# Optimization experiments

Hardware: AMD Instinct MI355X
Metric: run time of the kernel (lower is better)

## Reference

```python
import jax, jax.numpy as jnp
import numpy as np

B = 8
C = 256
N40, N20, N10 = 1600, 400, 100
N = N40 + N20 + N10  # 2100 pixel nodes (40x40 + 20x20 + 10x10)

def _grid_edges(h, w, off):
    # 8-neighborhood 'contextual' edges within one scale's grid
    idx = np.arange(h * w).reshape(h, w)
    srcs, dsts = [], []
    for di in (-1, 0, 1):
        for dj in (-1, 0, 1):
            if di == 0 and dj == 0:
                continue
            s = idx[max(0, -di):h - max(0, di), max(0, -dj):w - max(0, dj)]
            d = idx[max(0, di):h - max(0, -di), max(0, dj):w - max(0, -dj)]
            srcs.append(off + s.ravel())
            dsts.append(off + d.ravel())
    return srcs, dsts

def _hier_edges(ph, pw, poff, coff):
    # bidirected parent <-> 4-children 'hierarchical' edges between scales
    i, j = np.meshgrid(np.arange(ph), np.arange(pw), indexing='ij')
    parent = (poff + i * pw + j).ravel()
    srcs, dsts = [], []
    cw = 2 * pw
    for di in (0, 1):
        for dj in (0, 1):
            child = (coff + (2 * i + di) * cw + (2 * j + dj)).ravel()
            srcs += [parent, child]
            dsts += [child, parent]
    return srcs, dsts

def build_edges():
    loop = [np.arange(N)]  # dgl.add_self_loop on both etypes
    cs, cd = [], []
    for (h, w, off) in ((40, 40, 0), (20, 20, N40), (10, 10, N40 + N20)):
        s, d = _grid_edges(h, w, off)
        cs += s; cd += d
    ctx_src = np.concatenate(cs + loop); ctx_dst = np.concatenate(cd + loop)
    hs, hd = [], []
    s, d = _hier_edges(20, 20, N40, 0); hs += s; hd += d
    s, d = _hier_edges(10, 10, N40 + N20, N40); hs += s; hd += d
    hier_src = np.concatenate(hs + loop); hier_dst = np.concatenate(hd + loop)
    return (jnp.asarray(ctx_src, jnp.int32), jnp.asarray(ctx_dst, jnp.int32),
            jnp.asarray(hier_src, jnp.int32), jnp.asarray(hier_dst, jnp.int32))

def _bn_relu(x, g, b, m, v):
    # inference-mode BatchNorm2d + ReLU
    scale = g * jax.lax.rsqrt(v + 1e-5)
    return jax.nn.relu(x * scale[:, None, None] + (b - m * scale)[:, None, None])

def _conv1x1(x, w, b):
    return jnp.einsum('bchw,oc->bohw', x, w) + b[:, None, None]

def _avgpool2(x):
    b, c, h, w = x.shape
    return x.reshape(b, c, h // 2, 2, w // 2, 2).mean(axis=(3, 5))

def _up2(x):
    return jnp.repeat(jnp.repeat(x, 2, axis=2), 2, axis=3)

def _gnn(h, src, dst, deg_inv, w, b):
    # gather -> scatter-add -> mean over in-neighbors (incl. self loop) -> linear -> ReLU
    agg = jnp.zeros_like(h).at[:, dst].add(h[:, src]) * deg_inv[None, :, None]
    return jax.nn.relu(jnp.einsum('bnc,cd->bnd', agg, w) + b)

def _convT2x2(x, wt, b):
    # stride-2 2x2 transposed conv; wt: [Cin, Cout, 2, 2] (torch layout)
    bsz, cin, h, w = x.shape
    y = jnp.einsum('bchw,cokl->bohkwl', x, wt)
    return y.reshape(bsz, wt.shape[1], 2 * h, 2 * w) + b[:, None, None]

def setup_inputs():
    key = jax.random.key(0)
    ks = iter(jax.random.split(key, 64))
    def rn(shape, scale=0.02):
        return jax.random.normal(next(ks), shape, jnp.float32) * scale
    inp = {}
    inp['feat0'] = rn((B, 256, 160, 160), 1.0)
    inp['feat1'] = rn((B, 512, 80, 80), 1.0)
    inp['feat2'] = rn((B, 1024, 40, 40), 1.0)
    inp['feat3'] = rn((B, 2048, 20, 20), 1.0)
    for i, cin in ((1, 512), (2, 1024), (3, 2048)):
        inp['dw%d' % i] = rn((256, cin))
        inp['db%d' % i] = jnp.zeros((256,), jnp.float32)
        inp['g%d' % i] = jnp.ones((256,), jnp.float32)
        inp['b%d' % i] = jnp.zeros((256,), jnp.float32)
        inp['m%d' % i] = jnp.zeros((256,), jnp.float32)
        inp['v%d' % i] = jnp.ones((256,), jnp.float32)
    for i in range(1, 7):
        inp['gW%d' % i] = rn((256, 256))
        inp['gb%d' % i] = jnp.zeros((256,), jnp.float32)
    for i, cout in ((1, 512), (2, 1024), (3, 2048)):
        inp['tW%d' % i] = rn((256, cout, 2, 2))
        inp['tb%d' % i] = jnp.zeros((cout,), jnp.float32)
    ctx_src, ctx_dst, hier_src, hier_dst = build_edges()
    inp['ctx_src'] = ctx_src; inp['ctx_dst'] = ctx_dst
    inp['hier_src'] = hier_src; inp['hier_dst'] = hier_dst
    return inp

def reference(feat0, feat1, feat2, feat3,
              dw1, db1, g1, b1, m1, v1,
              dw2, db2, g2, b2, m2, v2,
              dw3, db3, g3, b3, m3, v3,
              gW1, gb1, gW2, gb2, gW3, gb3, gW4, gb4, gW5, gb5, gW6, gb6,
              tW1, tb1, tW2, tb2, tW3, tb3,
              ctx_src, ctx_dst, hier_src, hier_dst):
    f40 = _avgpool2(_bn_relu(_conv1x1(feat1, dw1, db1), g1, b1, m1, v1))  # [B,256,40,40]
    f20 = _avgpool2(_bn_relu(_conv1x1(feat2, dw2, db2), g2, b2, m2, v2))  # [B,256,20,20]
    f10 = _avgpool2(_bn_relu(_conv1x1(feat3, dw3, db3), g3, b3, m3, v3))  # [B,256,10,10]
    bsz = f40.shape[0]
    # cnn_gnn: flatten all three scales into [B, 2100, 256] node features (batched
    # version of the original per-sample python loop; graph is identical per sample)
    h = jnp.concatenate([
        f40.reshape(bsz, C, N40).transpose(0, 2, 1),
        f20.reshape(bsz, C, N20).transpose(0, 2, 1),
        f10.reshape(bsz, C, N10).transpose(0, 2, 1)], axis=1)
    dic = 1.0 / jnp.zeros((N,), h.dtype).at[ctx_dst].add(1.0)
    dih = 1.0 / jnp.zeros((N,), h.dtype).at[hier_dst].add(1.0)
    # context1, context2, hierarch1, hierarch2, context4, context5
    h = _gnn(h, ctx_src, ctx_dst, dic, gW1, gb1)
    h = _gnn(h, ctx_src, ctx_dst, dic, gW2, gb2)
    h = _gnn(h, hier_src, hier_dst, dih, gW3, gb3)
    h = _gnn(h, hier_src, hier_dst, dih, gW4, gb4)
    h = _gnn(h, ctx_src, ctx_dst, dic, gW5, gb5)
    h = _gnn(h, ctx_src, ctx_dst, dic, gW6, gb6)
    # gnn_cnn: split back to NCHW maps
    f40g = h[:, :N40].transpose(0, 2, 1).reshape(bsz, C, 40, 40)
    f20g = h[:, N40:N40 + N20].transpose(0, 2, 1).reshape(bsz, C, 20, 20)
    f10g = h[:, N40 + N20:].transpose(0, 2, 1).reshape(bsz, C, 10, 10)
    f10_ref = f10 + f10g
    f20_ref = f20 + f20g + _up2(f10g)
    f40_ref = f40 + f40g + _up2(f20g)
    out1 = _convT2x2(f40_ref, tW1, tb1) + feat1
    out2 = _convT2x2(f20_ref, tW2, tb2) + feat2
    out3 = _convT2x2(f10_ref, tW3, tb3) + feat3
    return (feat0, out1, out2, out3)
```

## Files before the change

### kernel.cpp

```cpp
#include <hip/hip_runtime.h>
#include <cstdint>

#define NODES 2100

typedef __attribute__((ext_vector_type(8))) __bf16 bf16x8;
typedef __attribute__((ext_vector_type(4))) float f32x4;
typedef __attribute__((ext_vector_type(8))) unsigned short u16x8;

__device__ inline float bf2f(unsigned short s) { return __uint_as_float(((unsigned)s) << 16); }
__device__ inline unsigned short f2bf(float f) {
    unsigned u = __float_as_uint(f);
    u += 0x7fff + ((u >> 16) & 1);
    return (unsigned short)(u >> 16);
}
__device__ inline void gload16(const unsigned short* g, void* lds) {
    __builtin_amdgcn_global_load_lds(
        (const __attribute__((address_space(1))) void*)g,
        (__attribute__((address_space(3))) void*)lds, 16, 0, 0);
}

__device__ __attribute__((always_inline)) inline
void gemm_core(const unsigned short* __restrict__ A, const unsigned short* __restrict__ B,
               int K, int m0, int n0, int mClamp, int nClamp,
               unsigned short* As, unsigned short* Bs, f32x4 acc[4][4])
{
    const int t = threadIdx.x, lane = t & 63, w = t >> 6;
    const int wr = w >> 1, wc = w & 1;
    const int sx = (lane & 7) << 4;
    for (int k0 = 0; k0 < K; k0 += 64) {
#pragma unroll
        for (int i = 0; i < 4; ++i) {
            int LO  = ((i << 8) + t) << 4;
            int row = LO >> 7;
            int kb  = (LO & 127) ^ ((row & 7) << 4);
            int ke  = kb >> 1;
            int ra = m0 + row; if (ra > mClamp) ra = mClamp;
            int rb = n0 + row; if (rb > nClamp) rb = nClamp;
            gload16(A + (size_t)ra * K + k0 + ke, (char*)As + LO);
            gload16(B + (size_t)rb * K + k0 + ke, (char*)Bs + LO);
        }
        asm volatile("s_waitcnt vmcnt(0)" ::: "memory");
        __syncthreads();
#pragma unroll
        for (int kk = 0; kk < 2; ++kk) {
            bf16x8 a[4], bb[4];
#pragma unroll
            for (int f = 0; f < 4; ++f) {
                int pa = (((wr * 64 + f * 16 + (lane & 15)) << 7) + kk * 64 + ((lane >> 4) << 4)) ^ sx;
                int pb = (((wc * 64 + f * 16 + (lane & 15)) << 7) + kk * 64 + ((lane >> 4) << 4)) ^ sx;
                a[f]  = *(const bf16x8*)((const char*)As + pa);
                bb[f] = *(const bf16x8*)((const char*)Bs + pb);
            }
#pragma unroll
            for (int fr = 0; fr < 4; ++fr)
#pragma unroll
                for (int fc = 0; fc < 4; ++fc)
                    acc[fr][fc] = __builtin_amdgcn_mfma_f32_16x16x32_bf16(a[fr], bb[fc], acc[fr][fc], 0, 0, 0);
        }
        __syncthreads();
    }
}

struct PrepArgs {
    const float *dw0, *dw1, *dw2;
    const float *gw0, *gw1, *gw2, *gw3, *gw4, *gw5;
    const float *tw0, *tw1, *tw2;
    const float *g0, *g1, *g2, *b0, *b1, *b2, *m0, *m1, *m2, *v0, *v1, *v2, *db0, *db1, *db2;
    unsigned short *dwb, *gWTb, *tWTb;
    float *scshb;
};

__device__ inline void transpose32(const float* __restrict__ in, unsigned short* __restrict__ outT,
                                   int Ccols, int c0, int r0)
{
    __shared__ float T[32][33];
    const int tx = threadIdx.x & 31, ty = threadIdx.x >> 5;
#pragma unroll
    for (int i = 0; i < 4; ++i)
        T[ty + i * 8][tx] = in[(size_t)(r0 + ty + i * 8) * Ccols + c0 + tx];
    __syncthreads();
#pragma unroll
    for (int i = 0; i < 4; ++i)
        outT[(size_t)(c0 + ty + i * 8) * 256 + r0 + tx] = f2bf(T[tx][ty + i * 8]);
}

__global__ __launch_bounds__(256)
void mega_prep(PrepArgs a)
{
    const int bid = blockIdx.x, t = threadIdx.x;
    if (bid < 448) {
        int idx = (bid * 256 + t) * 8;
        const float* src;
        int loc;
        if (idx < 131072)      { src = a.dw0; loc = idx; }
        else if (idx < 393216) { src = a.dw1; loc = idx - 131072; }
        else                   { src = a.dw2; loc = idx - 393216; }
        float4 x = *(const float4*)(src + loc);
        float4 y = *(const float4*)(src + loc + 4);
        u16x8 r;
        r[0] = f2bf(x.x); r[1] = f2bf(x.y); r[2] = f2bf(x.z); r[3] = f2bf(x.w);
        r[4] = f2bf(y.x); r[5] = f2bf(y.y); r[6] = f2bf(y.z); r[7] = f2bf(y.w);
        *(u16x8*)(a.dwb + idx) = r;
    } else if (bid < 832) {
        int gid = bid - 448;
        int l = gid >> 6, sb = gid & 63;
        const float* gw[6] = {a.gw0, a.gw1, a.gw2, a.gw3, a.gw4, a.gw5};
        transpose32(gw[l], a.gWTb + (size_t)l * 65536, 256, (sb & 7) << 5, (sb >> 3) << 5);
    } else if (bid < 4416) {
        int gid = bid - 832;
        const float* tw; unsigned short* dst; int ncx, loc;
        if (gid < 512)       { tw = a.tw0; dst = a.tWTb;           ncx = 64;  loc = gid; }
        else if (gid < 1536) { tw = a.tw1; dst = a.tWTb + 524288;  ncx = 128; loc = gid - 512; }
        else                 { tw = a.tw2; dst = a.tWTb + 1572864; ncx = 256; loc = gid - 1536; }
        int cx = loc % ncx, ry = loc / ncx;
        transpose32(tw, dst, ncx * 32, cx << 5, ry << 5);
    } else {
        const float* g[3]  = {a.g0, a.g1, a.g2};
        const float* b[3]  = {a.b0, a.b1, a.b2};
        const float* m[3]  = {a.m0, a.m1, a.m2};
        const float* v[3]  = {a.v0, a.v1, a.v2};
        const float* db[3] = {a.db0, a.db1, a.db2};
        for (int s = 0; s < 3; ++s) {
            float sc = g[s][t] * rsqrtf(v[s][t] + 1e-5f);
            a.scshb[s * 512 + t] = sc;
            a.scshb[s * 512 + 256 + t] = (db[s][t] - m[s][t]) * sc + b[s][t];
        }
    }
}

struct ConvArgs {
    const float* feat[3];
    const unsigned short* dwb[3];
    const float* scsh[3];
    unsigned short* h0out;
};

__global__ __launch_bounds__(256)
void conv_fused(ConvArgs ca)
{
    __shared__ __align__(16) unsigned short As[64 * 64];
    __shared__ __align__(16) unsigned short Bs[256 * 64];
    int bx = blockIdx.x;
    int s, mt;
    if (bx < 800)       { s = 0; mt = bx; }
    else if (bx < 1000) { s = 1; mt = bx - 800; }
    else                { s = 2; mt = bx - 1000; }
    const int Kc[3]  = {512, 1024, 2048};
    const int Wc[3]  = {80, 40, 20};
    const int PPc[3] = {1600, 400, 100};
    const int nfc[3] = {0, 1600, 2000};
    const int K = Kc[s], W = Wc[s], W2 = W >> 1, HW = W * W, PP = PPc[s], noff = nfc[s];
    const float* feat = ca.feat[s];
    const unsigned short* dw = ca.dwb[s];
    const float* scsh = ca.scsh[s];

    const int t = threadIdx.x, lane = t & 63, w = t >> 6;
    const int sx = (lane & 7) << 4;

    const int ml = t & 63;
    const int kw = t >> 6;
    const int graw = mt * 64 + ml;
    const int b = graw / HW;
    const int rem = graw - b * HW;
    const int pooled = rem >> 2, sub = rem & 3;
    const int pi = pooled / W2, pj = pooled - pi * W2;
    const int i = pi * 2 + (sub >> 1), j = pj * 2 + (sub & 1);
    const float* src = feat + (size_t)b * K * HW + (size_t)i * W + j;
    const int sxm = (ml & 7) << 3;

    f32x4 acc[4][4];
#pragma unroll
    for (int fr = 0; fr < 4; ++fr)
#pragma unroll
        for (int fc = 0; fc < 4; ++fc) acc[fr][fc] = (f32x4){0.f, 0.f, 0.f, 0.f};

    for (int k0 = 0; k0 < K; k0 += 64) {
#pragma unroll
        for (int it = 0; it < 8; ++it) {
            int LO = ((it << 8) + t) << 4;
            int row = LO >> 7;
            int kb = (LO & 127) ^ ((row & 7) << 4);
            gload16(dw + (size_t)row * K + k0 + (kb >> 1), (char*)Bs + LO);
        }
        float v[16];
#pragma unroll
        for (int it = 0; it < 16; ++it)
            v[it] = src[(size_t)(k0 + it * 4 + kw) * HW];
#pragma unroll
        for (int it = 0; it < 16; ++it) {
            int k_l = it * 4 + kw;
            As[(ml << 6) + (k_l ^ sxm)] = f2bf(v[it]);
        }
        asm volatile("s_waitcnt vmcnt(0)" ::: "memory");
        __syncthreads();
#pragma unroll
        for (int kk = 0; kk < 2; ++kk) {
            bf16x8 a[4], bb[4];
#pragma unroll
            for (int f = 0; f < 4; ++f) {
                int pa = (((f * 16 + (lane & 15)) << 7) + kk * 64 + ((lane >> 4) << 4)) ^ sx;
                int pb = (((w * 64 + f * 16 + (lane & 15)) << 7) + kk * 64 + ((lane >> 4) << 4)) ^ sx;
                a[f]  = *(const bf16x8*)((const char*)As + pa);
                bb[f] = *(const bf16x8*)((const char*)Bs + pb);
            }
#pragma unroll
            for (int fr = 0; fr < 4; ++fr)
#pragma unroll
                for (int fc = 0; fc < 4; ++fc)
                    acc[fr][fc] = __builtin_amdgcn_mfma_f32_16x16x32_bf16(a[fr], bb[fc], acc[fr][fc], 0, 0, 0);
        }
        __syncthreads();
    }

#pragma unroll
    for (int fc = 0; fc < 4; ++fc) {
        const int o = w * 64 + fc * 16 + (lane & 15);
        const float sc = scsh[o], sh = scsh[256 + o];
#pragma unroll
        for (int fr = 0; fr < 4; ++fr) {
            const int mrow = mt * 64 + fr * 16 + (lane >> 4) * 4;
            const int q = mrow >> 2;
            const int bi = q / PP;
            const int node = noff + (q - bi * PP);
            float sum = 0.f;
#pragma unroll
            for (int r = 0; r < 4; ++r)
                sum += fmaxf(acc[fr][fc][r] * sc + sh, 0.f);
            ca.h0out[((size_t)(bi * NODES + node)) * 256 + o] = f2bf(sum * 0.25f);
        }
    }
}

__global__ __launch_bounds__(256)
void gnn_fused(const unsigned short* __restrict__ h, const unsigned short* __restrict__ BT,
               const float* __restrict__ bias, unsigned short* __restrict__ out, int hier)
{
    __shared__ __align__(16) unsigned short As[32 * 64];
    __shared__ __align__(16) unsigned short Bs[256 * 64];
    const int t = threadIdx.x, lane = t & 63, w = t >> 6;
    const int r0 = blockIdx.x << 5;
    const int myrow = t >> 3, q = t & 7;
    const int grow = r0 + myrow;
    const int b = grow / NODES;
    const int n = grow - b * NODES;

    int gw, off;
    if (n < 1600)      { gw = 40; off = 0; }
    else if (n < 2000) { gw = 20; off = 1600; }
    else               { gw = 10; off = 2000; }
    const int li = (n - off) / gw;
    const int lj = (n - off) - li * gw;
    int nbr[9]; int cnt = 0;
    if (!hier) {
#pragma unroll
        for (int di = -1; di <= 1; ++di)
#pragma unroll
            for (int dj = -1; dj <= 1; ++dj) {
                int ii = li + di, jj = lj + dj;
                if (ii >= 0 && ii < gw && jj >= 0 && jj < gw) nbr[cnt++] = off + ii * gw + jj;
            }
    } else {
        nbr[cnt++] = n;
        if (off == 0) {
            nbr[cnt++] = 1600 + (li >> 1) * 20 + (lj >> 1);
        } else if (off == 1600) {
            nbr[cnt++] = 2000 + (li >> 1) * 10 + (lj >> 1);
#pragma unroll
            for (int di = 0; di < 2; ++di)
#pragma unroll
                for (int dj = 0; dj < 2; ++dj)
                    nbr[cnt++] = ((li << 1) + di) * 40 + ((lj << 1) + dj);
        } else {
#pragma unroll
            for (int di = 0; di < 2; ++di)
#pragma unroll
                for (int dj = 0; dj < 2; ++dj)
                    nbr[cnt++] = 1600 + ((li << 1) + di) * 20 + ((lj << 1) + dj);
        }
    }
    int nboff[9];
#pragma unroll
    for (int e = 0; e < 9; ++e)
        nboff[e] = (b * NODES + nbr[e < cnt ? e : 0]) * 256 + q * 8;
    const float inv = 1.0f / (float)cnt;
    const int sx = (lane & 7) << 4;
    const int awr = (myrow << 6) + ((q ^ (myrow & 7)) << 3);

    f32x4 acc[2][4];
#pragma unroll
    for (int fr = 0; fr < 2; ++fr)
#pragma unroll
        for (int fc = 0; fc < 4; ++fc) acc[fr][fc] = (f32x4){0.f, 0.f, 0.f, 0.f};

    for (int k0 = 0; k0 < 256; k0 += 64) {
#pragma unroll
        for (int it = 0; it < 8; ++it) {
            int LO = ((it << 8) + t) << 4;
            int row = LO >> 7;
            int kb = (LO & 127) ^ ((row & 7) << 4);
            gload16(BT + (size_t)row * 256 + k0 + (kb >> 1), (char*)Bs + LO);
        }
        float sacc[8] = {0, 0, 0, 0, 0, 0, 0, 0};
        for (int e = 0; e < cnt; ++e) {
            u16x8 vv = *(const u16x8*)(h + nboff[e] + k0);
#pragma unroll
            for (int jj = 0; jj < 8; ++jj) sacc[jj] += bf2f(vv[jj]);
        }
        u16x8 o0;
#pragma unroll
        for (int jj = 0; jj < 8; ++jj) o0[jj] = f2bf(sacc[jj] * inv);
        *(u16x8*)&As[awr] = o0;

        asm volatile("s_waitcnt vmcnt(0)" ::: "memory");
        __syncthreads();
#pragma unroll
        for (int kk = 0; kk < 2; ++kk) {
            bf16x8 a[2], bb[4];
#pragma unroll
            for (int f = 0; f < 2; ++f) {
                int pa = (((f * 16 + (lane & 15)) << 7) + kk * 64 + ((lane >> 4) << 4)) ^ sx;
                a[f] = *(const bf16x8*)((const char*)As + pa);
            }
#pragma unroll
            for (int f = 0; f < 4; ++f) {
                int pb = (((w * 64 + f * 16 + (lane & 15)) << 7) + kk * 64 + ((lane >> 4) << 4)) ^ sx;
                bb[f] = *(const bf16x8*)((const char*)Bs + pb);
            }
#pragma unroll
            for (int fr = 0; fr < 2; ++fr)
#pragma unroll
                for (int fc = 0; fc < 4; ++fc)
                    acc[fr][fc] = __builtin_amdgcn_mfma_f32_16x16x32_bf16(a[fr], bb[fc], acc[fr][fc], 0, 0, 0);
        }
        __syncthreads();
    }

#pragma unroll
    for (int fc = 0; fc < 4; ++fc) {
        const int d = w * 64 + fc * 16 + (lane & 15);
        const float bv = bias[d];
#pragma unroll
        for (int fr = 0; fr < 2; ++fr) {
            int rb = r0 + fr * 16 + (lane >> 4) * 4;
#pragma unroll
            for (int r = 0; r < 4; ++r)
                out[(size_t)(rb + r) * 256 + d] = f2bf(fmaxf(acc[fr][fc][r] + bv, 0.f));
        }
    }
}

__global__ __launch_bounds__(256)
void a_build(const unsigned short* __restrict__ h0, const unsigned short* __restrict__ h6,
             unsigned short* __restrict__ Ao)
{
    int bx = blockIdx.x;
    int P, H2, noff, pbase, pw, haspar; size_t aoff;
    if (bx < 1600)      { P = 1600; H2 = 40; noff = 0;    pbase = 1600; pw = 20; haspar = 1; aoff = 0; }
    else if (bx < 2000) { P = 400;  H2 = 20; noff = 1600; pbase = 2000; pw = 10; haspar = 1; aoff = 12800ULL * 256; bx -= 1600; }
    else                { P = 100;  H2 = 10; noff = 2000; pbase = 0;    pw = 0;  haspar = 0; aoff = 16000ULL * 256; bx -= 2000; }
    const int gid = bx * 256 + threadIdx.x;
    const int m = gid >> 5, c0 = (gid & 31) << 3;
    const int b = m / P, pix = m - b * P;
    const size_t src = ((size_t)(b * NODES + noff + pix)) * 256 + c0;
    u16x8 x0 = *(const u16x8*)(h0 + src);
    u16x8 x6 = *(const u16x8*)(h6 + src);
    float v[8];
#pragma unroll
    for (int e = 0; e < 8; ++e) v[e] = bf2f(x0[e]) + bf2f(x6[e]);
    if (haspar) {
        int ii = pix / H2, jj = pix - ii * H2;
        size_t sp = ((size_t)(b * NODES + pbase + (ii >> 1) * pw + (jj >> 1))) * 256 + c0;
        u16x8 xp = *(const u16x8*)(h6 + sp);
#pragma unroll
        for (int e = 0; e < 8; ++e) v[e] += bf2f(xp[e]);
    }
    u16x8 r;
#pragma unroll
    for (int e = 0; e < 8; ++e) r[e] = f2bf(v[e]);
    *(u16x8*)(Ao + aoff + (size_t)m * 256 + c0) = r;
}

struct ConvtArgs {
    const unsigned short* WT[3];
    const unsigned short* Apix[3];
    const float* tb[3];
    const float* feat[3];
    float* out[3];
};

__global__ __launch_bounds__(256)
void convt_fused(ConvtArgs ct)
{
    __shared__ __align__(16) unsigned short As[8192], Bs[8192];
    int bx = blockIdx.x;
    int s, px, my;
    if (bx < 1600)      { s = 0; px = bx % 100; my = bx / 100; }
    else if (bx < 2400) { s = 1; bx -= 1600; px = bx % 25; my = bx / 25; }
    else                { s = 2; bx -= 2400; px = bx % 7;  my = bx / 7; }
    const int Pc[3]  = {1600, 400, 100};
    const int H2c[3] = {40, 20, 10};
    const int Cc[3]  = {512, 1024, 2048};
    const int Mc[3]  = {12800, 3200, 800};
    const int P = Pc[s], H2 = H2c[s], Cout = Cc[s], Mpix = Mc[s];
    const int m0 = my << 7, n0 = px << 7;

    f32x4 acc[4][4];
#pragma unroll
    for (int fr = 0; fr < 4; ++fr)
#pragma unroll
        for (int fc = 0; fc < 4; ++fc) acc[fr][fc] = (f32x4){0.f, 0.f, 0.f, 0.f};

    gemm_core(ct.WT[s], ct.Apix[s], 256, m0, n0, Cout * 4 - 1, Mpix - 1, As, Bs, acc);

    const int lane = threadIdx.x & 63, w = threadIdx.x >> 6;
    const int wr = w >> 1, wc = w & 1;
    const int H = H2 * 2;
    const float* feat = ct.feat[s];
    float* out = ct.out[s];
#pragma unroll
    for (int fc = 0; fc < 4; ++fc) {
        const int p_g = n0 + wc * 64 + fc * 16 + (lane & 15);
        if (p_g < Mpix) {
            const int b = p_g / P, pix = p_g - b * P;
            const int ii = pix / H2, jj = pix - ii * H2;
#pragma unroll
            for (int fr = 0; fr < 4; ++fr) {
                const int rb = m0 + wr * 64 + fr * 16 + (lane >> 4) * 4;
                const int o = rb >> 2;
                const float tbo = ct.tb[s][o];
                size_t base = (((size_t)(b * Cout + o)) * H + 2 * ii) * H + 2 * jj;
                float2 f0 = *(const float2*)&feat[base];
                float2 r0v; r0v.x = acc[fr][fc][0] + tbo + f0.x; r0v.y = acc[fr][fc][1] + tbo + f0.y;
                *(float2*)&out[base] = r0v;
                float2 f1 = *(const float2*)&feat[base + H];
                float2 r1v; r1v.x = acc[fr][fc][2] + tbo + f1.x; r1v.y = acc[fr][fc][3] + tbo + f1.y;
                *(float2*)&out[base + H] = r1v;
            }
        }
    }
}

extern "C" void kernel_launch(void* const* d_in, const int* in_sizes, int n_in,
                              void* d_out, int out_size, void* d_ws, size_t ws_size,
                              hipStream_t stream)
{
    const float* feats[3] = { (const float*)d_in[1], (const float*)d_in[2], (const float*)d_in[3] };
    const float* gb[6];
    for (int l = 0; l < 6; ++l) gb[l] = (const float*)d_in[23 + 2 * l];
    const float* tb[3] = { (const float*)d_in[35], (const float*)d_in[37], (const float*)d_in[39] };

    size_t off = 0;
    auto alloc = [&](size_t bytes) { size_t r = off; off = (off + bytes + 511) & ~(size_t)511; return r; };
    unsigned short* h0b  = (unsigned short*)((char*)d_ws + alloc(16800ULL * 256 * 2));
    unsigned short* hA   = (unsigned short*)((char*)d_ws + alloc(16800ULL * 256 * 2));
    unsigned short* hB   = (unsigned short*)((char*)d_ws + alloc(16800ULL * 256 * 2));
    unsigned short* dwb  = (unsigned short*)((char*)d_ws + alloc(917504ULL * 2));
    unsigned short* gWTb = (unsigned short*)((char*)d_ws + alloc(6ULL * 65536 * 2));
    unsigned short* tWTb = (unsigned short*)((char*)d_ws + alloc(3670016ULL * 2));
    float*          scshb= (float*)((char*)d_ws + alloc(3ULL * 512 * 4));
    unsigned short* Aconvt = (unsigned short*)((char*)d_ws + off);

    hipMemcpyAsync(d_out, d_in[0], 52428800ULL * 4, hipMemcpyDeviceToDevice, stream);

    PrepArgs pa;
    pa.dw0 = (const float*)d_in[4];  pa.dw1 = (const float*)d_in[10]; pa.dw2 = (const float*)d_in[16];
    pa.gw0 = (const float*)d_in[22]; pa.gw1 = (const float*)d_in[24]; pa.gw2 = (const float*)d_in[26];
    pa.gw3 = (const float*)d_in[28]; pa.gw4 = (const float*)d_in[30]; pa.gw5 = (const float*)d_in[32];
    pa.tw0 = (const float*)d_in[34]; pa.tw1 = (const float*)d_in[36]; pa.tw2 = (const float*)d_in[38];
    pa.g0 = (const float*)d_in[6];  pa.g1 = (const float*)d_in[12]; pa.g2 = (const float*)d_in[18];
    pa.b0 = (const float*)d_in[7];  pa.b1 = (const float*)d_in[13]; pa.b2 = (const float*)d_in[19];
    pa.m0 = (const float*)d_in[8];  pa.m1 = (const float*)d_in[14]; pa.m2 = (const float*)d_in[20];
    pa.v0 = (const float*)d_in[9];  pa.v1 = (const float*)d_in[15]; pa.v2 = (const float*)d_in[21];
    pa.db0 = (const float*)d_in[5]; pa.db1 = (const float*)d_in[11]; pa.db2 = (const float*)d_in[17];
    pa.dwb = dwb; pa.gWTb = gWTb; pa.tWTb = tWTb; pa.scshb = scshb;
    mega_prep<<<dim3(4417), dim3(256), 0, stream>>>(pa);

    ConvArgs ca;
    ca.feat[0] = feats[0]; ca.feat[1] = feats[1]; ca.feat[2] = feats[2];
    ca.dwb[0] = dwb; ca.dwb[1] = dwb + 131072; ca.dwb[2] = dwb + 393216;
    ca.scsh[0] = scshb; ca.scsh[1] = scshb + 512; ca.scsh[2] = scshb + 1024;
    ca.h0out = h0b;
    conv_fused<<<dim3(1050), dim3(256), 0, stream>>>(ca);

    const int types[6] = {0, 0, 1, 1, 0, 0};
    const unsigned short* hin = h0b;
    unsigned short* houts[6] = {hA, hB, hA, hB, hA, hB};
    for (int l = 0; l < 6; ++l) {
        gnn_fused<<<dim3(525), dim3(256), 0, stream>>>(hin, gWTb + (size_t)l * 65536, gb[l], houts[l], types[l]);
        hin = houts[l];
    }
    unsigned short* h6 = hB;

    a_build<<<dim3(2100), dim3(256), 0, stream>>>(h0b, h6, Aconvt);

    ConvtArgs ct;
    ct.WT[0] = tWTb; ct.WT[1] = tWTb + 524288; ct.WT[2] = tWTb + 1572864;
    ct.Apix[0] = Aconvt; ct.Apix[1] = Aconvt + 12800ULL * 256; ct.Apix[2] = Aconvt + 16000ULL * 256;
    ct.tb[0] = tb[0]; ct.tb[1] = tb[1]; ct.tb[2] = tb[2];
    ct.feat[0] = feats[0]; ct.feat[1] = feats[1]; ct.feat[2] = feats[2];
    ct.out[0] = (float*)d_out + 52428800;
    ct.out[1] = (float*)d_out + 52428800 + 26214400;
    ct.out[2] = (float*)d_out + 52428800 + 26214400 + 13107200;
    convt_fused<<<dim3(2848), dim3(256), 0, stream>>>(ct);
}
```

Measured before the change: 500.4 us.

## Split feat0 passthrough copy across compute kernels and prefetch GNN neighbor rows

Replaces the 200MB device-to-device memcpy with eight 26MB chunks, each copied by extra blocks prepended to the prep, conv and six GNN kernels. The aim is to hide the bandwidth-bound copy behind compute-bound or latency-bound kernels instead of running it serially. The GNN kernel also prefetches all nine neighbor vectors for the next K-slice into registers before the MFMA loop, overlapping gather latency with compute. The cost is extra register pressure and copy blocks that compete for memory bandwidth and CUs with the existing work.

```diff
diff --git a/kernel.cpp b/kernel.cpp
--- a/kernel.cpp
+++ b/kernel.cpp
@@ -17,6 +17,12 @@
     __builtin_amdgcn_global_load_lds(
         (const __attribute__((address_space(1))) void*)g,
         (__attribute__((address_space(3))) void*)lds, 16, 0, 0);
+}
+
+__device__ inline void copy_chunk(const float4* __restrict__ s, float4* __restrict__ d,
+                                  int nquads, int bid, int nb)
+{
+    for (int i = bid * 256 + threadIdx.x; i < nquads; i += nb * 256) d[i] = s[i];
 }
 
 __device__ __attribute__((always_inline)) inline
@@ -68,6 +74,7 @@
     const float *g0, *g1, *g2, *b0, *b1, *b2, *m0, *m1, *m2, *v0, *v1, *v2, *db0, *db1, *db2;
     unsigned short *dwb, *gWTb, *tWTb;
     float *scshb;
+    const float4 *cps; float4 *cpd;
 };
 
 __device__ inline void transpose32(const float* __restrict__ in, unsigned short* __restrict__ outT,
@@ -87,7 +94,10 @@
 __global__ __launch_bounds__(256)
 void mega_prep(PrepArgs a)
 {
-    const int bid = blockIdx.x, t = threadIdx.x;
+    int bid = blockIdx.x;
+    const int t = threadIdx.x;
+    if (bid < 512) { copy_chunk(a.cps, a.cpd, 1638400, bid, 512); return; }
+    bid -= 512;
     if (bid < 448) {
         int idx = (bid * 256 + t) * 8;
         const float* src;
@@ -133,6 +143,7 @@
     const unsigned short* dwb[3];
     const float* scsh[3];
     unsigned short* h0out;
+    const float4 *cps; float4 *cpd;
 };
 
 __global__ __launch_bounds__(256)
@@ -141,6 +152,8 @@
     __shared__ __align__(16) unsigned short As[64 * 64];
     __shared__ __align__(16) unsigned short Bs[256 * 64];
     int bx = blockIdx.x;
+    if (bx < 128) { copy_chunk(ca.cps, ca.cpd, 1638400, bx, 128); return; }
+    bx -= 128;
     int s, mt;
     if (bx < 800)       { s = 0; mt = bx; }
     else if (bx < 1000) { s = 1; mt = bx - 800; }
@@ -233,12 +246,16 @@
 
 __global__ __launch_bounds__(256)
 void gnn_fused(const unsigned short* __restrict__ h, const unsigned short* __restrict__ BT,
-               const float* __restrict__ bias, unsigned short* __restrict__ out, int hier)
+               const float* __restrict__ bias, unsigned short* __restrict__ out, int hier,
+               const float4* __restrict__ cps, float4* __restrict__ cpd)
 {
     __shared__ __align__(16) unsigned short As[32 * 64];
     __shared__ __align__(16) unsigned short Bs[256 * 64];
+    int bx = blockIdx.x;
+    if (bx < 128) { copy_chunk(cps, cpd, 1638400, bx, 128); return; }
+    bx -= 128;
     const int t = threadIdx.x, lane = t & 63, w = t >> 6;
-    const int r0 = blockIdx.x << 5;
+    const int r0 = bx << 5;
     const int myrow = t >> 3, q = t & 7;
     const int grow = r0 + myrow;
     const int b = grow / NODES;
@@ -292,6 +309,10 @@
 #pragma unroll
         for (int fc = 0; fc < 4; ++fc) acc[fr][fc] = (f32x4){0.f, 0.f, 0.f, 0.f};
 
+    u16x8 pre[9];
+#pragma unroll
+    for (int e = 0; e < 9; ++e) pre[e] = *(const u16x8*)(h + nboff[e]);
+
     for (int k0 = 0; k0 < 256; k0 += 64) {
 #pragma unroll
         for (int it = 0; it < 8; ++it) {
@@ -301,10 +322,12 @@
             gload16(BT + (size_t)row * 256 + k0 + (kb >> 1), (char*)Bs + LO);
         }
         float sacc[8] = {0, 0, 0, 0, 0, 0, 0, 0};
-        for (int e = 0; e < cnt; ++e) {
-            u16x8 vv = *(const u16x8*)(h + nboff[e] + k0);
-#pragma unroll
-            for (int jj = 0; jj < 8; ++jj) sacc[jj] += bf2f(vv[jj]);
+#pragma unroll
+        for (int e = 0; e < 9; ++e) {
+            if (e < cnt) {
+#pragma unroll
+                for (int jj = 0; jj < 8; ++jj) sacc[jj] += bf2f(pre[e][jj]);
+            }
         }
         u16x8 o0;
 #pragma unroll
@@ -313,6 +336,11 @@
 
         asm volatile("s_waitcnt vmcnt(0)" ::: "memory");
         __syncthreads();
+
+        const int k0n = (k0 + 64) & 255;
+#pragma unroll
+        for (int e = 0; e < 9; ++e) pre[e] = *(const u16x8*)(h + nboff[e] + k0n);
+
 #pragma unroll
         for (int kk = 0; kk < 2; ++kk) {
             bf16x8 a[2], bb[4];
@@ -460,7 +488,9 @@
     float*          scshb= (float*)((char*)d_ws + alloc(3ULL * 512 * 4));
     unsigned short* Aconvt = (unsigned short*)((char*)d_ws + off);
 
-    hipMemcpyAsync(d_out, d_in[0], 52428800ULL * 4, hipMemcpyDeviceToDevice, stream);
+    const float4* f0s = (const float4*)d_in[0];
+    float4* f0d = (float4*)d_out;
+    const int CHK = 1638400;
 
     PrepArgs pa;
     pa.dw0 = (const float*)d_in[4];  pa.dw1 = (const float*)d_in[10]; pa.dw2 = (const float*)d_in[16];
@@ -473,20 +503,24 @@
     pa.v0 = (const float*)d_in[9];  pa.v1 = (const float*)d_in[15]; pa.v2 = (const float*)d_in[21];
     pa.db0 = (const float*)d_in[5]; pa.db1 = (const float*)d_in[11]; pa.db2 = (const float*)d_in[17];
     pa.dwb = dwb; pa.gWTb = gWTb; pa.tWTb = tWTb; pa.scshb = scshb;
-    mega_prep<<<dim3(4417), dim3(256), 0, stream>>>(pa);
+    pa.cps = f0s; pa.cpd = f0d;
+    mega_prep<<<dim3(512 + 4417), dim3(256), 0, stream>>>(pa);
 
     ConvArgs ca;
     ca.feat[0] = feats[0]; ca.feat[1] = feats[1]; ca.feat[2] = feats[2];
     ca.dwb[0] = dwb; ca.dwb[1] = dwb + 131072; ca.dwb[2] = dwb + 393216;
     ca.scsh[0] = scshb; ca.scsh[1] = scshb + 512; ca.scsh[2] = scshb + 1024;
     ca.h0out = h0b;
-    conv_fused<<<dim3(1050), dim3(256), 0, stream>>>(ca);
+    ca.cps = f0s + CHK; ca.cpd = f0d + CHK;
+    conv_fused<<<dim3(128 + 1050), dim3(256), 0, stream>>>(ca);
 
     const int types[6] = {0, 0, 1, 1, 0, 0};
     const unsigned short* hin = h0b;
     unsigned short* houts[6] = {hA, hB, hA, hB, hA, hB};
     for (int l = 0; l < 6; ++l) {
-        gnn_fused<<<dim3(525), dim3(256), 0, stream>>>(hin, gWTb + (size_t)l * 65536, gb[l], houts[l], types[l]);
+        gnn_fused<<<dim3(128 + 525), dim3(256), 0, stream>>>(
+            hin, gWTb + (size_t)l * 65536, gb[l], houts[l], types[l],
+            f0s + (size_t)(2 + l) * CHK, f0d + (size_t)(2 + l) * CHK);
         hin = houts[l];
     }
     unsigned short* h6 = hB;
```

Result: slower. 542.2 us (+8.3%).

## Fuse six GNN layers into one cooperative kernel and fold feat0 copy into convt

Applied to the files above, without the earlier changes.

Replaces six separate gnn_fused launches with one cooperative kernel of 512 blocks that loops over layers and uses grid.sync between them. It also prefetches the neighbor rows for the next K chunk into registers so the loads overlap the MFMA work. The 200MB feat0 device-to-device memcpy is removed and done instead by 512 extra blocks prepended to the convt_fused launch, so it can overlap the convt GEMM. The risks are grid-sync overhead, more register pressure from the prefetch buffers, and uneven work, since 525 strips over 512 blocks leaves a tail.

```diff
diff --git a/kernel.cpp b/kernel.cpp
--- a/kernel.cpp
+++ b/kernel.cpp
@@ -1,4 +1,5 @@
 #include <hip/hip_runtime.h>
+#include <hip/hip_cooperative_groups.h>
 #include <cstdint>
 
 #define NODES 2100
@@ -17,6 +18,12 @@
     __builtin_amdgcn_global_load_lds(
         (const __attribute__((address_space(1))) void*)g,
         (__attribute__((address_space(3))) void*)lds, 16, 0, 0);
+}
+
+__device__ inline void copy_chunk(const float4* __restrict__ s, float4* __restrict__ d,
+                                  int nquads, int bid, int nb)
+{
+    for (int i = bid * 256 + threadIdx.x; i < nquads; i += nb * 256) d[i] = s[i];
 }
 
 __device__ __attribute__((always_inline)) inline
@@ -87,7 +94,8 @@
 __global__ __launch_bounds__(256)
 void mega_prep(PrepArgs a)
 {
-    const int bid = blockIdx.x, t = threadIdx.x;
+    int bid = blockIdx.x;
+    const int t = threadIdx.x;
     if (bid < 448) {
         int idx = (bid * 256 + t) * 8;
         const float* src;
@@ -231,121 +239,155 @@
     }
 }
 
+struct GnnAllArgs {
+    const unsigned short* h0;
+    unsigned short* bufA;
+    unsigned short* bufB;
+    const unsigned short* WT;
+    const float *gb0, *gb1, *gb2, *gb3, *gb4, *gb5;
+};
+
 __global__ __launch_bounds__(256)
-void gnn_fused(const unsigned short* __restrict__ h, const unsigned short* __restrict__ BT,
-               const float* __restrict__ bias, unsigned short* __restrict__ out, int hier)
+void gnn_all(GnnAllArgs a)
 {
     __shared__ __align__(16) unsigned short As[32 * 64];
     __shared__ __align__(16) unsigned short Bs[256 * 64];
+    cooperative_groups::grid_group grid = cooperative_groups::this_grid();
     const int t = threadIdx.x, lane = t & 63, w = t >> 6;
-    const int r0 = blockIdx.x << 5;
-    const int myrow = t >> 3, q = t & 7;
-    const int grow = r0 + myrow;
-    const int b = grow / NODES;
-    const int n = grow - b * NODES;
-
-    int gw, off;
-    if (n < 1600)      { gw = 40; off = 0; }
-    else if (n < 2000) { gw = 20; off = 1600; }
-    else               { gw = 10; off = 2000; }
-    const int li = (n - off) / gw;
-    const int lj = (n - off) - li * gw;
-    int nbr[9]; int cnt = 0;
-    if (!hier) {
-#pragma unroll
-        for (int di = -1; di <= 1; ++di)
-#pragma unroll
-            for (int dj = -1; dj <= 1; ++dj) {
-                int ii = li + di, jj = lj + dj;
-                if (ii >= 0 && ii < gw && jj >= 0 && jj < gw) nbr[cnt++] = off + ii * gw + jj;
+    const int sx = (lane & 7) << 4;
+    const unsigned short* hin = a.h0;
+
+    for (int l = 0; l < 6; ++l) {
+        unsigned short* out = (l & 1) ? a.bufB : a.bufA;
+        const unsigned short* BT = a.WT + (size_t)l * 65536;
+        const float* bias = (l == 0) ? a.gb0 : (l == 1) ? a.gb1 : (l == 2) ? a.gb2
+                          : (l == 3) ? a.gb3 : (l == 4) ? a.gb4 : a.gb5;
+        const int hier = (l == 2 || l == 3);
+
+        for (int strip = blockIdx.x; strip < 525; strip += gridDim.x) {
+            const int r0 = strip << 5;
+            const int myrow = t >> 3, q = t & 7;
+            const int grow = r0 + myrow;
+            const int b = grow / NODES;
+            const int n = grow - b * NODES;
+
+            int gw, off;
+            if (n < 1600)      { gw = 40; off = 0; }
+            else if (n < 2000) { gw = 20; off = 1600; }
+            else               { gw = 10; off = 2000; }
+            const int li = (n - off) / gw;
+            const int lj = (n - off) - li * gw;
+            int nbr[9]; int cnt = 0;
+            if (!hier) {
+#pragma unroll
+                for (int di = -1; di <= 1; ++di)
+#pragma unroll
+                    for (int dj = -1; dj <= 1; ++dj) {
+                        int ii = li + di, jj = lj + dj;
+                        if (ii >= 0 && ii < gw && jj >= 0 && jj < gw) nbr[cnt++] = off + ii * gw + jj;
+                    }
+            } else {
+                nbr[cnt++] = n;
+                if (off == 0) {
+                    nbr[cnt++] = 1600 + (li >> 1) * 20 + (lj >> 1);
+                } else if (off == 1600) {
+                    nbr[cnt++] = 2000 + (li >> 1) * 10 + (lj >> 1);
+#pragma unroll
+                    for (int di = 0; di < 2; ++di)
+#pragma unroll
+                        for (int dj = 0; dj < 2; ++dj)
+                            nbr[cnt++] = ((li << 1) + di) * 40 + ((lj << 1) + dj);
+                } else {
+#pragma unroll
+                    for (int di = 0; di < 2; ++di)
+#pragma unroll
+                        for (int dj = 0; dj < 2; ++dj)
+                            nbr[cnt++] = 1600 + ((li << 1) + di) * 20 + ((lj << 1) + dj);
+                }
             }
-    } else {
-        nbr[cnt++] = n;
-        if (off == 0) {
-            nbr[cnt++] = 1600 + (li >> 1) * 20 + (lj >> 1);
-        } else if (off == 1600) {
-            nbr[cnt++] = 2000 + (li >> 1) * 10 + (lj >> 1);
-#pragma unroll
-            for (int di = 0; di < 2; ++di)
-#pragma unroll
-                for (int dj = 0; dj < 2; ++dj)
-                    nbr[cnt++] = ((li << 1) + di) * 40 + ((lj << 1) + dj);
-        } else {
-#pragma unroll
-            for (int di = 0; di < 2; ++di)
-#pragma unroll
-                for (int dj = 0; dj < 2; ++dj)
-                    nbr[cnt++] = 1600 + ((li << 1) + di) * 20 + ((lj << 1) + dj);
-        }
-    }
-    int nboff[9];
-#pragma unroll
-    for (int e = 0; e < 9; ++e)
-        nboff[e] = (b * NODES + nbr[e < cnt ? e : 0]) * 256 + q * 8;
-    const float inv = 1.0f / (float)cnt;
-    const int sx = (lane & 7) << 4;
-    const int awr = (myrow << 6) + ((q ^ (myrow & 7)) << 3);
-
-    f32x4 acc[2][4];
-#pragma unroll
-    for (int fr = 0; fr < 2; ++fr)
-#pragma unroll
-        for (int fc = 0; fc < 4; ++fc) acc[fr][fc] = (f32x4){0.f, 0.f, 0.f, 0.f};
-
-    for (int k0 = 0; k0 < 256; k0 += 64) {
-#pragma unroll
-        for (int it = 0; it < 8; ++it) {
-            int LO = ((it << 8) + t) << 4;
-            int row = LO >> 7;
-            int kb = (LO & 127) ^ ((row & 7) << 4);
-            gload16(BT + (size_t)row * 256 + k0 + (kb >> 1), (char*)Bs + LO);
-        }
-        float sacc[8] = {0, 0, 0, 0, 0, 0, 0, 0};
-        for (int e = 0; e < cnt; ++e) {
-            u16x8 vv = *(const u16x8*)(h + nboff[e] + k0);
-#pragma unroll
-            for (int jj = 0; jj < 8; ++jj) sacc[jj] += bf2f(vv[jj]);
-        }
-        u16x8 o0;
-#pragma unroll
-        for (int jj = 0; jj < 8; ++jj) o0[jj] = f2bf(sacc[jj] * inv);
-        *(u16x8*)&As[awr] = o0;
-
-        asm volatile("s_waitcnt vmcnt(0)" ::: "memory");
-        __syncthreads();
-#pragma unroll
-        for (int kk = 0; kk < 2; ++kk) {
-            bf16x8 a[2], bb[4];
-#pragma unroll
-            for (int f = 0; f < 2; ++f) {
-                int pa = (((f * 16 + (lane & 15)) << 7) + kk * 64 + ((lane >> 4) << 4)) ^ sx;
-                a[f] = *(const bf16x8*)((const char*)As + pa);
+            int nboff[9];
+#pragma unroll
+            for (int e = 0; e < 9; ++e)
+                nboff[e] = (b * NODES + nbr[e < cnt ? e : 0]) * 256 + q * 8;
+            const float inv = 1.0f / (float)cnt;
+            const int awr = (myrow << 6) + ((q ^ (myrow & 7)) << 3);
+
+            f32x4 acc[2][4];
+#pragma unroll
+            for (int fr = 0; fr < 2; ++fr)
+#pragma unroll
+                for (int fc = 0; fc < 4; ++fc) acc[fr][fc] = (f32x4){0.f, 0.f, 0.f, 0.f};
+
+            u16x8 pre[9];
+#pragma unroll
+            for (int e = 0; e < 9; ++e) pre[e] = *(const u16x8*)(hin + nboff[e]);
+
+            for (int k0 = 0; k0 < 256; k0 += 64) {
+#pragma unroll
+                for (int it = 0; it < 8; ++it) {
+                    int LO = ((it << 8) + t) << 4;
+                    int row = LO >> 7;
+                    int kb = (LO & 127) ^ ((row & 7) << 4);
+                    gload16(BT + (size_t)row * 256 + k0 + (kb >> 1), (char*)Bs + LO);
+                }
+                float sacc[8] = {0, 0, 0, 0, 0, 0, 0, 0};
+#pragma unroll
+                for (int e = 0; e < 9; ++e) {
+                    if (e < cnt) {
+#pragma unroll
+                        for (int jj = 0; jj < 8; ++jj) sacc[jj] += bf2f(pre[e][jj]);
+                    }
+                }
+                u16x8 o0;
+#pragma unroll
+                for (int jj = 0; jj < 8; ++jj) o0[jj] = f2bf(sacc[jj] * inv);
+                *(u16x8*)&As[awr] = o0;
+
+                asm volatile("s_waitcnt vmcnt(0)" ::: "memory");
+                __syncthreads();
+
+                const int k0n = (k0 + 64) & 255;
+#pragma unroll
+                for (int e = 0; e < 9; ++e) pre[e] = *(const u16x8*)(hin + nboff[e] + k0n);
+
+#pragma unroll
+                for (int kk = 0; kk < 2; ++kk) {
+                    bf16x8 av[2], bb[4];
+#pragma unroll
+                    for (int f = 0; f < 2; ++f) {
+                        int pa = (((f * 16 + (lane & 15)) << 7) + kk * 64 + ((lane >> 4) << 4)) ^ sx;
+                        av[f] = *(const bf16x8*)((const char*)As + pa);
+                    }
+#pragma unroll
+                    for (int f = 0; f < 4; ++f) {
+                        int pb = (((w * 64 + f * 16 + (lane & 15)) << 7) + kk * 64 + ((lane >> 4) << 4)) ^ sx;
+                        bb[f] = *(const bf16x8*)((const char*)Bs + pb);
+                    }
+#pragma unroll
+                    for (int fr = 0; fr < 2; ++fr)
+#pragma unroll
+                        for (int fc = 0; fc < 4; ++fc)
+                            acc[fr][fc] = __builtin_amdgcn_mfma_f32_16x16x32_bf16(av[fr], bb[fc], acc[fr][fc], 0, 0, 0);
+                }
+                __syncthreads();
             }
-#pragma unroll
-            for (int f = 0; f < 4; ++f) {
-                int pb = (((w * 64 + f * 16 + (lane & 15)) << 7) + kk * 64 + ((lane >> 4) << 4)) ^ sx;
-                bb[f] = *(const bf16x8*)((const char*)Bs + pb);
+
+#pragma unroll
+            for (int fc = 0; fc < 4; ++fc) {
+                const int d = w * 64 + fc * 16 + (lane & 15);
+                const float bv = bias[d];
+#pragma unroll
+                for (int fr = 0; fr < 2; ++fr) {
+                    int rb = r0 + fr * 16 + (lane >> 4) * 4;
+#pragma unroll
+                    for (int r = 0; r < 4; ++r)
+                        out[(size_t)(rb + r) * 256 + d] = f2bf(fmaxf(acc[fr][fc][r] + bv, 0.f));
+                }
             }
-#pragma unroll
-            for (int fr = 0; fr < 2; ++fr)
-#pragma unroll
-                for (int fc = 0; fc < 4; ++fc)
-                    acc[fr][fc] = __builtin_amdgcn_mfma_f32_16x16x32_bf16(a[fr], bb[fc], acc[fr][fc], 0, 0, 0);
-        }
-        __syncthreads();
-    }
-
-#pragma unroll
-    for (int fc = 0; fc < 4; ++fc) {
-        const int d = w * 64 + fc * 16 + (lane & 15);
-        const float bv = bias[d];
-#pragma unroll
-        for (int fr = 0; fr < 2; ++fr) {
-            int rb = r0 + fr * 16 + (lane >> 4) * 4;
-#pragma unroll
-            for (int r = 0; r < 4; ++r)
-                out[(size_t)(rb + r) * 256 + d] = f2bf(fmaxf(acc[fr][fc][r] + bv, 0.f));
-        }
+        }
+        __threadfence();
+        grid.sync();
+        hin = out;
     }
 }
 
@@ -386,6 +428,7 @@
     const float* tb[3];
     const float* feat[3];
     float* out[3];
+    const float4* cps; float4* cpd;
 };
 
 __global__ __launch_bounds__(256)
@@ -393,6 +436,8 @@
 {
     __shared__ __align__(16) unsigned short As[8192], Bs[8192];
     int bx = blockIdx.x;
+    if (bx < 512) { copy_chunk(ct.cps, ct.cpd, 13107200, bx, 512); return; }
+    bx -= 512;
     int s, px, my;
     if (bx < 1600)      { s = 0; px = bx % 100; my = bx / 100; }
     else if (bx < 2400) { s = 1; bx -= 1600; px = bx % 25; my = bx / 25; }
@@ -445,8 +490,6 @@
                               hipStream_t stream)
 {
     const float* feats[3] = { (const float*)d_in[1], (const float*)d_in[2], (const float*)d_in[3] };
-    const float* gb[6];
-    for (int l = 0; l < 6; ++l) gb[l] = (const float*)d_in[23 + 2 * l];
     const float* tb[3] = { (const float*)d_in[35], (const float*)d_in[37], (const float*)d_in[39] };
 
     size_t off = 0;
@@ -459,8 +502,6 @@
     unsigned short* tWTb = (unsigned short*)((char*)d_ws + alloc(3670016ULL * 2));
     float*          scshb= (float*)((char*)d_ws + alloc(3ULL * 512 * 4));
     unsigned short* Aconvt = (unsigned short*)((char*)d_ws + off);
-
-    hipMemcpyAsync(d_out, d_in[0], 52428800ULL * 4, hipMemcpyDeviceToDevice, stream);
 
     PrepArgs pa;
     pa.dw0 = (const float*)d_in[4];  pa.dw1 = (const float*)d_in[10]; pa.dw2 = (const float*)d_in[16];
@@ -482,13 +523,14 @@
     ca.h0out = h0b;
     conv_fused<<<dim3(1050), dim3(256), 0, stream>>>(ca);
 
-    const int types[6] = {0, 0, 1, 1, 0, 0};
-    const unsigned short* hin = h0b;
-    unsigned short* houts[6] = {hA, hB, hA, hB, hA, hB};
-    for (int l = 0; l < 6; ++l) {
-        gnn_fused<<<dim3(525), dim3(256), 0, stream>>>(hin, gWTb + (size_t)l * 65536, gb[l], houts[l], types[l]);
-        hin = houts[l];
-    }
+    GnnAllArgs ga;
+    ga.h0 = h0b; ga.bufA = hA; ga.bufB = hB; ga.WT = gWTb;
+    ga.gb0 = (const float*)d_in[23]; ga.gb1 = (const float*)d_in[25];
+    ga.gb2 = (const float*)d_in[27]; ga.gb3 = (const float*)d_in[29];
+    ga.gb4 = (const float*)d_in[31]; ga.gb5 = (const float*)d_in[33];
+    void* kargs[] = { (void*)&ga };
+    hipLaunchCooperativeKernel(reinterpret_cast<void*>(gnn_all),
+                               dim3(512), dim3(256), kargs, 0, stream);
     unsigned short* h6 = hB;
 
     a_build<<<dim3(2100), dim3(256), 0, stream>>>(h0b, h6, Aconvt);
@@ -501,5 +543,7 @@
     ct.out[0] = (float*)d_out + 52428800;
     ct.out[1] = (float*)d_out + 52428800 + 26214400;
     ct.out[2] = (float*)d_out + 52428800 + 26214400 + 13107200;
-    convt_fused<<<dim3(2848), dim3(256), 0, stream>>>(ct);
-}
+    ct.cps = (const float4*)d_in[0];
+    ct.cpd = (float4*)d_out;
+    convt_fused<<<dim3(512 + 2848), dim3(256), 0, stream>>>(ct);
+}
```

Result: slower. 1.187 ms (+137.2%).

## Fold feat0 passthrough copy into convt kernel and prefetch GNN neighbor rows

Applied to the files above, without the earlier changes.

Drops the separate device-to-device memcpy of feat0 (about 210 MB) and has 512 extra blocks inside convt_fused do the copy, so it can overlap with the transposed-conv GEMM blocks. The GNN kernel also register-prefetches the next k-chunk of all 9 neighbor rows before the MFMA loop, which hides gather latency but adds registers and always issues 9 loads per chunk. The copy blocks compete with the GEMM blocks for bandwidth and CU slots.

```diff
diff --git a/kernel.cpp b/kernel.cpp
--- a/kernel.cpp
+++ b/kernel.cpp
@@ -17,6 +17,12 @@
     __builtin_amdgcn_global_load_lds(
         (const __attribute__((address_space(1))) void*)g,
         (__attribute__((address_space(3))) void*)lds, 16, 0, 0);
+}
+
+__device__ inline void copy_chunk(const float4* __restrict__ s, float4* __restrict__ d,
+                                  int nquads, int bid, int nb)
+{
+    for (int i = bid * 256 + threadIdx.x; i < nquads; i += nb * 256) d[i] = s[i];
 }
 
 __device__ __attribute__((always_inline)) inline
@@ -87,7 +93,8 @@
 __global__ __launch_bounds__(256)
 void mega_prep(PrepArgs a)
 {
-    const int bid = blockIdx.x, t = threadIdx.x;
+    int bid = blockIdx.x;
+    const int t = threadIdx.x;
     if (bid < 448) {
         int idx = (bid * 256 + t) * 8;
         const float* src;
@@ -292,6 +299,10 @@
 #pragma unroll
         for (int fc = 0; fc < 4; ++fc) acc[fr][fc] = (f32x4){0.f, 0.f, 0.f, 0.f};
 
+    u16x8 pre[9];
+#pragma unroll
+    for (int e = 0; e < 9; ++e) pre[e] = *(const u16x8*)(h + nboff[e]);
+
     for (int k0 = 0; k0 < 256; k0 += 64) {
 #pragma unroll
         for (int it = 0; it < 8; ++it) {
@@ -301,10 +312,12 @@
             gload16(BT + (size_t)row * 256 + k0 + (kb >> 1), (char*)Bs + LO);
         }
         float sacc[8] = {0, 0, 0, 0, 0, 0, 0, 0};
-        for (int e = 0; e < cnt; ++e) {
-            u16x8 vv = *(const u16x8*)(h + nboff[e] + k0);
-#pragma unroll
-            for (int jj = 0; jj < 8; ++jj) sacc[jj] += bf2f(vv[jj]);
+#pragma unroll
+        for (int e = 0; e < 9; ++e) {
+            if (e < cnt) {
+#pragma unroll
+                for (int jj = 0; jj < 8; ++jj) sacc[jj] += bf2f(pre[e][jj]);
+            }
         }
         u16x8 o0;
 #pragma unroll
@@ -313,6 +326,11 @@
 
         asm volatile("s_waitcnt vmcnt(0)" ::: "memory");
         __syncthreads();
+
+        const int k0n = (k0 + 64) & 255;
+#pragma unroll
+        for (int e = 0; e < 9; ++e) pre[e] = *(const u16x8*)(h + nboff[e] + k0n);
+
 #pragma unroll
         for (int kk = 0; kk < 2; ++kk) {
             bf16x8 a[2], bb[4];
@@ -386,6 +404,7 @@
     const float* tb[3];
     const float* feat[3];
     float* out[3];
+    const float4* cps; float4* cpd;
 };
 
 __global__ __launch_bounds__(256)
@@ -393,6 +412,8 @@
 {
     __shared__ __align__(16) unsigned short As[8192], Bs[8192];
     int bx = blockIdx.x;
+    if (bx < 512) { copy_chunk(ct.cps, ct.cpd, 13107200, bx, 512); return; }
+    bx -= 512;
     int s, px, my;
     if (bx < 1600)      { s = 0; px = bx % 100; my = bx / 100; }
     else if (bx < 2400) { s = 1; bx -= 1600; px = bx % 25; my = bx / 25; }
@@ -459,8 +480,6 @@
     unsigned short* tWTb = (unsigned short*)((char*)d_ws + alloc(3670016ULL * 2));
     float*          scshb= (float*)((char*)d_ws + alloc(3ULL * 512 * 4));
     unsigned short* Aconvt = (unsigned short*)((char*)d_ws + off);
-
-    hipMemcpyAsync(d_out, d_in[0], 52428800ULL * 4, hipMemcpyDeviceToDevice, stream);
 
     PrepArgs pa;
     pa.dw0 = (const float*)d_in[4];  pa.dw1 = (const float*)d_in[10]; pa.dw2 = (const float*)d_in[16];
@@ -486,7 +505,8 @@
     const unsigned short* hin = h0b;
     unsigned short* houts[6] = {hA, hB, hA, hB, hA, hB};
     for (int l = 0; l < 6; ++l) {
-        gnn_fused<<<dim3(525), dim3(256), 0, stream>>>(hin, gWTb + (size_t)l * 65536, gb[l], houts[l], types[l]);
+        gnn_fused<<<dim3(525), dim3(256), 0, stream>>>(
+            hin, gWTb + (size_t)l * 65536, gb[l], houts[l], types[l]);
         hin = houts[l];
     }
     unsigned short* h6 = hB;
@@ -501,5 +521,7 @@
     ct.out[0] = (float*)d_out + 52428800;
     ct.out[1] = (float*)d_out + 52428800 + 26214400;
     ct.out[2] = (float*)d_out + 52428800 + 26214400 + 13107200;
-    convt_fused<<<dim3(2848), dim3(256), 0, stream>>>(ct);
-}
+    ct.cps = (const float4*)d_in[0];
+    ct.cpd = (float4*)d_out;
+    convt_fused<<<dim3(512 + 2848), dim3(256), 0, stream>>>(ct);
+}
```

New measurement: 488.5 us. 2.4% less time.
